# Kernel tuning notes

Hardware: AMD Instinct MI355X
Metric: run time of the kernel (lower is better)

## Reference

```python
import jax, jax.numpy as jnp
import numpy as np

P = 5.0  # p-norm order from init_kwargs


def setup_inputs() -> dict:
    key = jax.random.key(0)
    k1, k2 = jax.random.split(key)
    B, N, M, C = 8, 4096, 4096, 3
    x = jax.random.normal(k1, (B, N, C), dtype=jnp.float32)
    y = jax.random.normal(k2, (B, M, C), dtype=jnp.float32)
    return {"x": x, "y": y}


def _pnorm(v, axis):
    # (sum |v|^p)^(1/p), matching torch.norm(p=5)
    return jnp.sum(jnp.abs(v) ** P, axis=axis) ** (1.0 / P)


def reference(x, y):
    # Squared Euclidean distance matrix [B, N, M]
    d = (-2.0 * jnp.einsum("bnc,bmc->bnm", x, y)
         + jnp.sum(x * x, -1)[:, :, None]
         + jnp.sum(y * y, -1)[:, None, :])
    idx1 = jnp.argmin(d, axis=2)  # [B, N]: nearest y for each x
    idx2 = jnp.argmin(d, axis=1)  # [B, M]: nearest x for each y
    nn_y = jnp.take_along_axis(y, idx1[..., None], axis=1)  # [B, N, 3]
    nn_x = jnp.take_along_axis(x, idx2[..., None], axis=1)  # [B, M, 3]
    pc1 = _pnorm(x - nn_y, axis=-1)  # [B, N]
    pc2 = _pnorm(y - nn_x, axis=-1)  # [B, M]
    result2 = _pnorm(pc1, axis=-1) + _pnorm(pc2, axis=-1)  # [B]
    return jnp.mean(result2)
```

## Files before the change

kernel.cpp:

```cpp
#include <hip/hip_runtime.h>
#include <math.h>


#define BQ      256
#define QPT     4
#define SPLITS  16
#define CH      256
#define GS      8
#define NG      (CH / GS)
#define BIGOFF  64.0f
#define NQTOT   65536
#define NTILE   64
#define TILEQ   1024

typedef float f32x2 __attribute__((ext_vector_type(2)));
typedef float f32x4 __attribute__((ext_vector_type(4)));

static __device__ __forceinline__ f32x2 mk2(float s) { f32x2 v; v.x = s; v.y = s; return v; }
static __device__ __forceinline__ f32x2 fma2(f32x2 a, f32x2 b, f32x2 c) {
    return __builtin_elementwise_fma(a, b, c);
}
__device__ __forceinline__ unsigned int float_ord(float f) {
    unsigned int u = __float_as_uint(f);
    return (u & 0x80000000u) ? ~u : (u | 0x80000000u);
}

#define WS_ACC    0
#define WS_CANARY 128
#define WS_GCNT   192
#define WS_TCNT   256
#define WS_PSUM   1024
#define WS_TAB    4096
#define WS_TBL    1048576

__global__ __launch_bounds__(BQ) void chamfer_mktab(
    const float* __restrict__ x, const float* __restrict__ y,
    float4* __restrict__ tbl)
{
    const int t   = blockIdx.x * BQ + threadIdx.x;
    const int dir = t >> 14;
    const int b   = (t >> 11) & 7;
    const int pr  = t & 2047;
    const float* R = (dir == 0 ? y : x) + (size_t)b * 4096 * 3;
    const float* rp = R + (size_t)(2 * pr) * 3;
    const float f0 = rp[0], f1 = rp[1], f2 = rp[2];
    const float f3 = rp[3], f4 = rp[4], f5 = rp[5];
    const float h0 = fmaf(0.5f * f0, f0, fmaf(0.5f * f1, f1, fmaf(0.5f * f2, f2, BIGOFF)));
    const float h1 = fmaf(0.5f * f3, f3, fmaf(0.5f * f4, f4, fmaf(0.5f * f5, f5, BIGOFF)));
    const size_t o = ((size_t)(dir * 8 + b) * 2048 + pr) * 2;
    tbl[o]     = make_float4(f0, f3, f1, f4);
    tbl[o + 1] = make_float4(f2, f5, h0, h1);
}

#define COMPUTE_GROUP(BUF, G)                                              \
  {                                                                        \
    float mloc[QPT];                                                       \
    _Pragma("unroll")                                                      \
    for (int k4 = 0; k4 < 4; ++k4) {                                       \
      const f32x4 a = BUF[2 * k4];                    \
      const f32x4 c = BUF[2 * k4 + 1];                 \
      const f32x2 rx = __builtin_shufflevector(a, a, 0, 1);                \
      const f32x2 ry = __builtin_shufflevector(a, a, 2, 3);                \
      const f32x2 rz = __builtin_shufflevector(c, c, 0, 1);                \
      const f32x2 h2 = __builtin_shufflevector(c, c, 2, 3);                \
      _Pragma("unroll")                                                    \
      for (int qk = 0; qk < QPT; ++qk) {                                   \
        const f32x2 s = fma2(nqx[qk], rx,                                  \
                        fma2(nqy[qk], ry, fma2(nqz[qk], rz, h2)));         \
        if (k4 == 0) mloc[qk] = fminf(s.x, s.y);                           \
        else         mloc[qk] = fminf(fminf(mloc[qk], s.x), s.y);          \
      }                                                                    \
    }                                                                      \
    _Pragma("unroll")                                                      \
    for (int qk = 0; qk < QPT; ++qk) {                                     \
      const bool cc = mloc[qk] < best[qk];   \
      best[qk] = cc ? mloc[qk] : best[qk];                                 \
      bg[qk]   = cc ? (G) : bg[qk];                                        \
    }                                                                      \
  }

__global__ __launch_bounds__(BQ, 4) void chamfer_fused_r14(
    const float* __restrict__ x, const float* __restrict__ y,
    const f32x4* __restrict__ tbl,
    unsigned long long* __restrict__ tab,
    unsigned int* __restrict__ tcnt, unsigned int* __restrict__ gcnt,
    const unsigned int* __restrict__ canary_p,
    float* __restrict__ psum, float* __restrict__ out)
{
    __shared__ float red[4];
    __shared__ int s_flag;

    const int bid   = blockIdx.x;
    const int split = bid & (SPLITS - 1);
    const int tq    = bid >> 4;
    const int dir   = tq >> 5;
    const int b     = (tq >> 2) & 7;
    const int t4    = tq & 3;

    const unsigned int canary = *canary_p;

    const float* Q; const float* R;
    if (dir == 0) { Q = x + (size_t)b * 4096 * 3; R = y + (size_t)b * 4096 * 3; }
    else          { Q = y + (size_t)b * 4096 * 3; R = x + (size_t)b * 4096 * 3; }

    const int tid = threadIdx.x;

    const f32x4* __restrict__ tb =
        tbl + ((size_t)(dir * 8 + b) * 4096 + (size_t)split * 256);

    f32x2 nqx[QPT], nqy[QPT], nqz[QPT];
    #pragma unroll
    for (int qk = 0; qk < QPT; ++qk) {
        const int ql = t4 * TILEQ + qk * 256 + tid;
        nqx[qk] = mk2(-Q[ql * 3 + 0]);
        nqy[qk] = mk2(-Q[ql * 3 + 1]);
        nqz[qk] = mk2(-Q[ql * 3 + 2]);
    }

    float best[QPT]; int bg[QPT];
    #pragma unroll
    for (int qk = 0; qk < QPT; ++qk) { best[qk] = 3.4e38f; bg[qk] = 0; }

    f32x4 bufA[8], bufB[8];
    #pragma unroll
    for (int i = 0; i < 8; ++i) bufA[i] = tb[i];

    #pragma unroll 1
    for (int g = 0; g < NG; g += 2) {
        #pragma unroll
        for (int i = 0; i < 8; ++i) bufB[i] = tb[(g + 1) * 8 + i];
        COMPUTE_GROUP(bufA, g)
        const int gpre = (g + 2) & (NG - 1);
        #pragma unroll
        for (int i = 0; i < 8; ++i) bufA[i] = tb[gpre * 8 + i];
        COMPUTE_GROUP(bufB, g + 1)
    }

    #pragma unroll
    for (int qk = 0; qk < QPT; ++qk) {
        const float bscore = best[qk];
        const float qx = -nqx[qk].x;
        const float qy = -nqy[qk].x;
        const float qz = -nqz[qk].x;
        const int basej = split * CH + bg[qk] * GS;
        int bj = basej;
        #pragma unroll
        for (int j = GS - 1; j >= 0; --j) {
            const float* rp = R + (size_t)(basej + j) * 3;
            const float rx = rp[0], ry = rp[1], rz = rp[2];
            const float h = fmaf(0.5f * rx, rx, fmaf(0.5f * ry, ry, fmaf(0.5f * rz, rz, BIGOFF)));
            const float s = fmaf(-qx, rx, fmaf(-qy, ry, fmaf(-qz, rz, h)));
            if (s == bscore) bj = basej + j;
        }
        const size_t qidx = (size_t)tq * TILEQ + qk * 256 + tid;
        const unsigned long long key =
            ~(((unsigned long long)__float_as_uint(bscore) << 32) | (unsigned int)bj);
        atomicMax(&tab[qidx], key);
    }

    __syncthreads();
    if (tid == 0) {
        const unsigned int old = atomicAdd(&tcnt[tq], 1u);
        s_flag = (old == canary + (SPLITS - 1));
    }
    __syncthreads();
    if (!s_flag) return;

    float sthr = 0.0f;
    #pragma unroll
    for (int k = 0; k < QPT; ++k) {
        const int gq = tq * TILEQ + k * 256 + tid;
        const int q  = t4 * TILEQ + k * 256 + tid;
        const unsigned long long w =
            ~__hip_atomic_load(&tab[gq], __ATOMIC_RELAXED, __HIP_MEMORY_SCOPE_AGENT);
        const int j = (int)(unsigned int)w;
        const float dx = Q[q * 3 + 0] - R[(size_t)j * 3 + 0];
        const float dy = Q[q * 3 + 1] - R[(size_t)j * 3 + 1];
        const float dz = Q[q * 3 + 2] - R[(size_t)j * 3 + 2];
        const float ax = fabsf(dx), ay = fabsf(dy), az = fabsf(dz);
        const float ax2 = ax * ax, ay2 = ay * ay, az2 = az * az;
        sthr += ax2 * ax2 * ax + ay2 * ay2 * ay + az2 * az2 * az;
    }
    #pragma unroll
    for (int off = 32; off > 0; off >>= 1) sthr += __shfl_down(sthr, off, 64);
    const int wid = tid >> 6, lane = tid & 63;
    if (lane == 0) red[wid] = sthr;
    __syncthreads();

    if (tid == 0) {
        __hip_atomic_store(&psum[tq], red[0] + red[1] + red[2] + red[3],
                           __ATOMIC_RELAXED, __HIP_MEMORY_SCOPE_AGENT);
        asm volatile("s_waitcnt vmcnt(0)" ::: "memory");
        const unsigned int old = atomicAdd(gcnt, 1u);
        s_flag = (old == canary + (NTILE - 1));
    }
    __syncthreads();
    if (!s_flag) return;

    if (tid < 64) {
        float v = 0.0f;
        if (tid < 16) {
            const int fb = tid >> 1, fdir = tid & 1;
            float a = 0.0f;
            #pragma unroll
            for (int t = 0; t < 4; ++t)
                a += __hip_atomic_load(&psum[fdir * 32 + fb * 4 + t],
                                       __ATOMIC_RELAXED, __HIP_MEMORY_SCOPE_AGENT);
            v = exp2f(0.2f * log2f(a));
        }
        #pragma unroll
        for (int off = 8; off > 0; off >>= 1) v += __shfl_down(v, off, 64);
        if (tid == 0) out[0] = v * 0.125f;
    }
    if (tid < NTILE)
        __hip_atomic_store(&tcnt[tid], canary, __ATOMIC_RELAXED, __HIP_MEMORY_SCOPE_AGENT);
    if (tid == 0)
        __hip_atomic_store(gcnt, canary, __ATOMIC_RELAXED, __HIP_MEMORY_SCOPE_AGENT);
}

__global__ __launch_bounds__(BQ) void chamfer_nn_split_kernel(
    const float* __restrict__ x, const float* __restrict__ y,
    unsigned long long* __restrict__ packed, int N, int M)
{
    __shared__ float4 sref[1024];
    const int bid = blockIdx.x, split = bid & 3, qb = bid >> 2;
    const int tile = qb & 15, dir = (qb >> 4) & 1, b = qb >> 5;
    const float* Q; const float* R;
    if (dir == 0) { Q = x + (size_t)b * N * 3; R = y + (size_t)b * M * 3; }
    else          { Q = y + (size_t)b * M * 3; R = x + (size_t)b * N * 3; }
    const int tid = threadIdx.x, q = tile * BQ + tid, base = split * 1024;
    for (int j = tid; j < 1024; j += BQ) {
        const float rx = R[(size_t)(base + j) * 3 + 0];
        const float ry = R[(size_t)(base + j) * 3 + 1];
        const float rz = R[(size_t)(base + j) * 3 + 2];
        sref[j] = make_float4(rx, ry, rz, 0.5f * (rx * rx + ry * ry + rz * rz));
    }
    __syncthreads();
    const float qx = Q[q * 3 + 0], qy = Q[q * 3 + 1], qz = Q[q * 3 + 2];
    float best = 3.4e38f; int bestj = base;
    #pragma unroll 8
    for (int j = 0; j < 1024; ++j) {
        const float4 r = sref[j];
        float t = __fmaf_rn(-qx, r.x, r.w);
        t = __fmaf_rn(-qy, r.y, t);
        t = __fmaf_rn(-qz, r.z, t);
        const bool c = t < best;
        best = c ? t : best; bestj = c ? (base + j) : bestj;
    }
    const size_t idx = ((size_t)dir * 8 + b) * (size_t)N + q;
    atomicMin(&packed[idx], ((unsigned long long)float_ord(best) << 32) | (unsigned int)bestj);
}

__global__ __launch_bounds__(BQ) void chamfer_gather_kernel(
    const float* __restrict__ x, const float* __restrict__ y,
    const unsigned long long* __restrict__ packed,
    float* __restrict__ acc, int N, int M)
{
    __shared__ float red[4];
    const int tid = threadIdx.x;
    const size_t gq = (size_t)blockIdx.x * BQ + tid;
    const int dir = (int)(gq / ((size_t)8 * N));
    const size_t rem = gq - (size_t)dir * 8 * N;
    const int b = (int)(rem / N), q = (int)(rem - (size_t)b * N);
    const float* Q; const float* R;
    if (dir == 0) { Q = x + (size_t)b * N * 3; R = y + (size_t)b * M * 3; }
    else          { Q = y + (size_t)b * M * 3; R = x + (size_t)b * N * 3; }
    const int j = (int)(unsigned int)packed[gq];
    const float dx = Q[q * 3 + 0] - R[(size_t)j * 3 + 0];
    const float dy = Q[q * 3 + 1] - R[(size_t)j * 3 + 1];
    const float dz = Q[q * 3 + 2] - R[(size_t)j * 3 + 2];
    const float ax = fabsf(dx), ay = fabsf(dy), az = fabsf(dz);
    const float ax2 = ax * ax, ay2 = ay * ay, az2 = az * az;
    float s = ax2 * ax2 * ax + ay2 * ay2 * ay + az2 * az2 * az;
    #pragma unroll
    for (int off = 32; off > 0; off >>= 1) s += __shfl_down(s, off, 64);
    const int wid = tid >> 6, lane = tid & 63;
    if (lane == 0) red[wid] = s;
    __syncthreads();
    if (tid == 0) atomicAdd(&acc[b * 2 + dir], red[0] + red[1] + red[2] + red[3]);
}

__global__ void chamfer_finalize_kernel(const float* __restrict__ acc,
                                        float* __restrict__ out)
{
    if (threadIdx.x == 0 && blockIdx.x == 0) {
        float total = 0.0f;
        #pragma unroll
        for (int i = 0; i < 16; ++i) total += powf(acc[i], 0.2f);
        *out = total * 0.125f;
    }
}

extern "C" void kernel_launch(void* const* d_in, const int* in_sizes, int n_in,
                              void* d_out, int out_size, void* d_ws, size_t ws_size,
                              hipStream_t stream)
{
    const float* x = (const float*)d_in[0];
    const float* y = (const float*)d_in[1];
    float* out = (float*)d_out;
    const int N = in_sizes[0] / 24;
    const int M = in_sizes[1] / 24;

    const size_t needed = WS_TBL + (1u << 20);

    if (N == 4096 && M == 4096 && ws_size >= needed) {
        unsigned char* ws = (unsigned char*)d_ws;
        unsigned long long* tab = (unsigned long long*)(ws + WS_TAB);
        unsigned int* tcnt = (unsigned int*)(ws + WS_TCNT);
        unsigned int* gcnt = (unsigned int*)(ws + WS_GCNT);
        const unsigned int* canary = (const unsigned int*)(ws + WS_CANARY);
        float* psum = (float*)(ws + WS_PSUM);
        chamfer_mktab<<<32768 / BQ, BQ, 0, stream>>>(x, y, (float4*)(ws + WS_TBL));
        chamfer_fused_r14<<<NTILE * SPLITS, BQ, 0, stream>>>(
            x, y, (const f32x4*)(ws + WS_TBL), tab, tcnt, gcnt, canary, psum, out);
    } else {
        unsigned char* ws = (unsigned char*)d_ws;
        float* acc = (float*)ws;
        unsigned long long* ptab = (unsigned long long*)(ws + 4096);
        const size_t nQ = (size_t)2 * 8 * N;
        hipMemsetAsync(acc, 0, 64, stream);
        hipMemsetAsync(ptab, 0xFF, nQ * 8, stream);
        chamfer_nn_split_kernel<<<(int)(nQ / BQ) * 4, BQ, 0, stream>>>(x, y, ptab, N, M);
        chamfer_gather_kernel<<<(int)(nQ / BQ), BQ, 0, stream>>>(x, y, ptab, acc, N, M);
        chamfer_finalize_kernel<<<1, 64, 0, stream>>>(acc, out);
    }
}
```

Baseline: 87.87 us.

## Load reference tiles via scalar s_load_dwordx16 and use packed min accumulation

Replaces the per-thread vector loads of uniform reference table entries (double-buffered f32x4 registers) with inline-asm scalar loads of two 16-dword blocks per group into SGPRs. Each group now waits for its loads to finish, so there is no software prefetch overlap. The per-group minimum is accumulated with a packed 2-wide min and reduced once at the end. The intent is to free VGPRs and vector memory bandwidth by using the scalar cache for wave-uniform data, at the cost of a full lgkmcnt stall every group.

```diff
diff --git a/kernel.cpp b/kernel.cpp
--- a/kernel.cpp
+++ b/kernel.cpp
@@ -13,12 +13,16 @@
 #define NTILE   64
 #define TILEQ   1024
 
-typedef float f32x2 __attribute__((ext_vector_type(2)));
-typedef float f32x4 __attribute__((ext_vector_type(4)));
+typedef float f32x2  __attribute__((ext_vector_type(2)));
+typedef float f32x4  __attribute__((ext_vector_type(4)));
+typedef float f32x16 __attribute__((ext_vector_type(16)));
 
 static __device__ __forceinline__ f32x2 mk2(float s) { f32x2 v; v.x = s; v.y = s; return v; }
 static __device__ __forceinline__ f32x2 fma2(f32x2 a, f32x2 b, f32x2 c) {
     return __builtin_elementwise_fma(a, b, c);
+}
+static __device__ __forceinline__ f32x2 min2(f32x2 a, f32x2 b) {
+    return __builtin_elementwise_min(a, b);
 }
 __device__ __forceinline__ unsigned int float_ord(float f) {
     unsigned int u = __float_as_uint(f);
@@ -52,36 +56,23 @@
     tbl[o + 1] = make_float4(f2, f5, h0, h1);
 }
 
-#define COMPUTE_GROUP(BUF, G)                                              \
-  {                                                                        \
-    float mloc[QPT];                                                       \
-    _Pragma("unroll")                                                      \
-    for (int k4 = 0; k4 < 4; ++k4) {                                       \
-      const f32x4 a = BUF[2 * k4];                    \
-      const f32x4 c = BUF[2 * k4 + 1];                 \
-      const f32x2 rx = __builtin_shufflevector(a, a, 0, 1);                \
-      const f32x2 ry = __builtin_shufflevector(a, a, 2, 3);                \
-      const f32x2 rz = __builtin_shufflevector(c, c, 0, 1);                \
-      const f32x2 h2 = __builtin_shufflevector(c, c, 2, 3);                \
-      _Pragma("unroll")                                                    \
-      for (int qk = 0; qk < QPT; ++qk) {                                   \
-        const f32x2 s = fma2(nqx[qk], rx,                                  \
-                        fma2(nqy[qk], ry, fma2(nqz[qk], rz, h2)));         \
-        if (k4 == 0) mloc[qk] = fminf(s.x, s.y);                           \
-        else         mloc[qk] = fminf(fminf(mloc[qk], s.x), s.y);          \
-      }                                                                    \
-    }                                                                      \
-    _Pragma("unroll")                                                      \
-    for (int qk = 0; qk < QPT; ++qk) {                                     \
-      const bool cc = mloc[qk] < best[qk];   \
-      best[qk] = cc ? mloc[qk] : best[qk];                                 \
-      bg[qk]   = cc ? (G) : bg[qk];                                        \
-    }                                                                      \
+#define PAIR_COMPUTE(W, B)                                               \
+  {                                                                      \
+    const f32x2 rx = __builtin_shufflevector(W, W, (B) + 0, (B) + 1);    \
+    const f32x2 ry = __builtin_shufflevector(W, W, (B) + 2, (B) + 3);    \
+    const f32x2 rz = __builtin_shufflevector(W, W, (B) + 4, (B) + 5);    \
+    const f32x2 h2 = __builtin_shufflevector(W, W, (B) + 6, (B) + 7);    \
+    _Pragma("unroll")                                                    \
+    for (int qk = 0; qk < QPT; ++qk) {                                   \
+      const f32x2 s = fma2(nqx[qk], rx,                                  \
+                      fma2(nqy[qk], ry, fma2(nqz[qk], rz, h2)));         \
+      macc[qk] = min2(macc[qk], s);               \
+    }                                                                    \
   }
 
-__global__ __launch_bounds__(BQ, 4) void chamfer_fused_r14(
+__global__ __launch_bounds__(BQ, 4) void chamfer_fused_r17(
     const float* __restrict__ x, const float* __restrict__ y,
-    const f32x4* __restrict__ tbl,
+    const float* __restrict__ tbl,
     unsigned long long* __restrict__ tab,
     unsigned int* __restrict__ tcnt, unsigned int* __restrict__ gcnt,
     const unsigned int* __restrict__ canary_p,
@@ -105,8 +96,7 @@
 
     const int tid = threadIdx.x;
 
-    const f32x4* __restrict__ tb =
-        tbl + ((size_t)(dir * 8 + b) * 4096 + (size_t)split * 256);
+    const float* tb = tbl + ((size_t)(dir * 8 + b) * 16384 + (size_t)split * 1024);
 
     f32x2 nqx[QPT], nqy[QPT], nqz[QPT];
     #pragma unroll
@@ -121,19 +111,32 @@
     #pragma unroll
     for (int qk = 0; qk < QPT; ++qk) { best[qk] = 3.4e38f; bg[qk] = 0; }
 
-    f32x4 bufA[8], bufB[8];
-    #pragma unroll
-    for (int i = 0; i < 8; ++i) bufA[i] = tb[i];
-
     #pragma unroll 1
-    for (int g = 0; g < NG; g += 2) {
-        #pragma unroll
-        for (int i = 0; i < 8; ++i) bufB[i] = tb[(g + 1) * 8 + i];
-        COMPUTE_GROUP(bufA, g)
-        const int gpre = (g + 2) & (NG - 1);
-        #pragma unroll
-        for (int i = 0; i < 8; ++i) bufA[i] = tb[gpre * 8 + i];
-        COMPUTE_GROUP(bufB, g + 1)
+    for (int g = 0; g < NG; ++g) {
+        f32x16 w0, w1;
+        const unsigned int goff = (unsigned int)(g * 128);
+        asm("s_load_dwordx16 %0, %2, %3\n\t"
+            "s_load_dwordx16 %1, %2, %4\n\t"
+            "s_waitcnt lgkmcnt(0)"
+            : "=s"(w0), "=s"(w1)
+            : "s"(tb), "s"(goff), "s"(goff + 64u));
+
+        f32x2 macc[QPT];
+        #pragma unroll
+        for (int qk = 0; qk < QPT; ++qk) macc[qk] = mk2(3.4e38f);
+
+        PAIR_COMPUTE(w0, 0)
+        PAIR_COMPUTE(w0, 8)
+        PAIR_COMPUTE(w1, 0)
+        PAIR_COMPUTE(w1, 8)
+
+        #pragma unroll
+        for (int qk = 0; qk < QPT; ++qk) {
+            const float m = fminf(macc[qk].x, macc[qk].y);
+            const bool cc = m < best[qk];
+            best[qk] = cc ? m : best[qk];
+            bg[qk]   = cc ? g : bg[qk];
+        }
     }
 
     #pragma unroll
@@ -311,8 +314,8 @@
         const unsigned int* canary = (const unsigned int*)(ws + WS_CANARY);
         float* psum = (float*)(ws + WS_PSUM);
         chamfer_mktab<<<32768 / BQ, BQ, 0, stream>>>(x, y, (float4*)(ws + WS_TBL));
-        chamfer_fused_r14<<<NTILE * SPLITS, BQ, 0, stream>>>(
-            x, y, (const f32x4*)(ws + WS_TBL), tab, tcnt, gcnt, canary, psum, out);
+        chamfer_fused_r17<<<NTILE * SPLITS, BQ, 0, stream>>>(
+            x, y, (const float*)(ws + WS_TBL), tab, tcnt, gcnt, canary, psum, out);
     } else {
         unsigned char* ws = (unsigned char*)d_ws;
         float* acc = (float*)ws;
```

New measurement: 88.02 us. No clear change (+0.2%).

## Fuse reference-table build into main kernel via shared-memory staging

Applied to the files above, without the earlier changes.

Drops the separate table-building kernel launch. Each block now builds its own 256-point reference chunk (coordinates plus half-norm offset) directly into shared memory, and the inner loop reads that staging instead of a global workspace table. This removes one launch and its global round trip, and turns the inner-loop reads into LDS broadcasts. The cost is that every block redoes the preprocessing for its chunk and pays an extra barrier before the main loop.

```diff
diff --git a/kernel.cpp b/kernel.cpp
--- a/kernel.cpp
+++ b/kernel.cpp
@@ -31,26 +31,6 @@
 #define WS_TCNT   256
 #define WS_PSUM   1024
 #define WS_TAB    4096
-#define WS_TBL    1048576
-
-__global__ __launch_bounds__(BQ) void chamfer_mktab(
-    const float* __restrict__ x, const float* __restrict__ y,
-    float4* __restrict__ tbl)
-{
-    const int t   = blockIdx.x * BQ + threadIdx.x;
-    const int dir = t >> 14;
-    const int b   = (t >> 11) & 7;
-    const int pr  = t & 2047;
-    const float* R = (dir == 0 ? y : x) + (size_t)b * 4096 * 3;
-    const float* rp = R + (size_t)(2 * pr) * 3;
-    const float f0 = rp[0], f1 = rp[1], f2 = rp[2];
-    const float f3 = rp[3], f4 = rp[4], f5 = rp[5];
-    const float h0 = fmaf(0.5f * f0, f0, fmaf(0.5f * f1, f1, fmaf(0.5f * f2, f2, BIGOFF)));
-    const float h1 = fmaf(0.5f * f3, f3, fmaf(0.5f * f4, f4, fmaf(0.5f * f5, f5, BIGOFF)));
-    const size_t o = ((size_t)(dir * 8 + b) * 2048 + pr) * 2;
-    tbl[o]     = make_float4(f0, f3, f1, f4);
-    tbl[o + 1] = make_float4(f2, f5, h0, h1);
-}
 
 #define COMPUTE_GROUP(BUF, G)                                              \
   {                                                                        \
@@ -79,14 +59,14 @@
     }                                                                      \
   }
 
-__global__ __launch_bounds__(BQ, 4) void chamfer_fused_r14(
+__global__ __launch_bounds__(BQ, 4) void chamfer_fused_r19(
     const float* __restrict__ x, const float* __restrict__ y,
-    const f32x4* __restrict__ tbl,
     unsigned long long* __restrict__ tab,
     unsigned int* __restrict__ tcnt, unsigned int* __restrict__ gcnt,
     const unsigned int* __restrict__ canary_p,
     float* __restrict__ psum, float* __restrict__ out)
 {
+    __shared__ f32x4 sref[CH];
     __shared__ float red[4];
     __shared__ int s_flag;
 
@@ -105,8 +85,17 @@
 
     const int tid = threadIdx.x;
 
-    const f32x4* __restrict__ tb =
-        tbl + ((size_t)(dir * 8 + b) * 4096 + (size_t)split * 256);
+    if (tid < CH / 2) {
+        const float* rp = R + (size_t)(split * CH + 2 * tid) * 3;
+        const float f0 = rp[0], f1 = rp[1], f2 = rp[2];
+        const float f3 = rp[3], f4 = rp[4], f5 = rp[5];
+        const float h0 = fmaf(0.5f * f0, f0, fmaf(0.5f * f1, f1, fmaf(0.5f * f2, f2, BIGOFF)));
+        const float h1 = fmaf(0.5f * f3, f3, fmaf(0.5f * f4, f4, fmaf(0.5f * f5, f5, BIGOFF)));
+        f32x4 e0; e0.x = f0; e0.y = f3; e0.z = f1; e0.w = f4;
+        f32x4 e1; e1.x = f2; e1.y = f5; e1.z = h0; e1.w = h1;
+        sref[2 * tid]     = e0;
+        sref[2 * tid + 1] = e1;
+    }
 
     f32x2 nqx[QPT], nqy[QPT], nqz[QPT];
     #pragma unroll
@@ -116,6 +105,7 @@
         nqy[qk] = mk2(-Q[ql * 3 + 1]);
         nqz[qk] = mk2(-Q[ql * 3 + 2]);
     }
+    __syncthreads();
 
     float best[QPT]; int bg[QPT];
     #pragma unroll
@@ -123,16 +113,16 @@
 
     f32x4 bufA[8], bufB[8];
     #pragma unroll
-    for (int i = 0; i < 8; ++i) bufA[i] = tb[i];
+    for (int i = 0; i < 8; ++i) bufA[i] = sref[i];
 
     #pragma unroll 1
     for (int g = 0; g < NG; g += 2) {
         #pragma unroll
-        for (int i = 0; i < 8; ++i) bufB[i] = tb[(g + 1) * 8 + i];
+        for (int i = 0; i < 8; ++i) bufB[i] = sref[(g + 1) * 8 + i];
         COMPUTE_GROUP(bufA, g)
         const int gpre = (g + 2) & (NG - 1);
         #pragma unroll
-        for (int i = 0; i < 8; ++i) bufA[i] = tb[gpre * 8 + i];
+        for (int i = 0; i < 8; ++i) bufA[i] = sref[gpre * 8 + i];
         COMPUTE_GROUP(bufB, g + 1)
     }
 
@@ -301,7 +291,7 @@
     const int N = in_sizes[0] / 24;
     const int M = in_sizes[1] / 24;
 
-    const size_t needed = WS_TBL + (1u << 20);
+    const size_t needed = WS_TAB + (size_t)NQTOT * 8;
 
     if (N == 4096 && M == 4096 && ws_size >= needed) {
         unsigned char* ws = (unsigned char*)d_ws;
@@ -310,9 +300,8 @@
         unsigned int* gcnt = (unsigned int*)(ws + WS_GCNT);
         const unsigned int* canary = (const unsigned int*)(ws + WS_CANARY);
         float* psum = (float*)(ws + WS_PSUM);
-        chamfer_mktab<<<32768 / BQ, BQ, 0, stream>>>(x, y, (float4*)(ws + WS_TBL));
-        chamfer_fused_r14<<<NTILE * SPLITS, BQ, 0, stream>>>(
-            x, y, (const f32x4*)(ws + WS_TBL), tab, tcnt, gcnt, canary, psum, out);
+        chamfer_fused_r19<<<NTILE * SPLITS, BQ, 0, stream>>>(
+            x, y, tab, tcnt, gcnt, canary, psum, out);
     } else {
         unsigned char* ws = (unsigned char*)d_ws;
         float* acc = (float*)ws;
```

New measurement: 86.18 us. Within noise of the previous version (-1.9%).
